# Optimization experiments

Measured on AMD Instinct MI355X. Metric: run time of the kernel, lower is better.

## Reference

```python
import jax, jax.numpy as jnp
import numpy as np

MARGIN = 0.2


def setup_inputs() -> dict:
    key = jax.random.key(0)
    ks = jax.random.split(key, 6)
    B, E = 8192, 1024
    return {
        "A_is_t": jax.random.normal(ks[0], (B, E), dtype=jnp.float32),
        "A_em_t": jax.random.normal(ks[1], (B, E), dtype=jnp.float32),
        "m": jax.random.normal(ks[2], (B, E), dtype=jnp.float32),
        "tr_m": jax.random.normal(ks[3], (B, E), dtype=jnp.float32),
        "W": jax.random.normal(ks[4], (E, E), dtype=jnp.float32) * (1.0 / np.sqrt(E)),
        "b": jax.random.normal(ks[5], (E,), dtype=jnp.float32) * 0.01,
    }


def reference(A_is_t, A_em_t, m, tr_m, W, b):
    # Linear layer: w(A) = A @ W.T + b  (torch nn.Linear convention)
    wA_is = A_is_t @ W.T + b  # [B, E]
    wA_em = A_em_t @ W.T + b  # [B, E]
    # Original builds full [B,B] score matrices but only uses the diagonal;
    # diagonal entries are exactly rowwise dots, computed directly here.
    d_is = jnp.einsum("be,be->b", m, wA_is)
    d_em = jnp.einsum("be,be->b", m, wA_em)
    d_is_trm = jnp.einsum("be,be->b", tr_m, wA_is)
    d_em_trm = jnp.einsum("be,be->b", tr_m, wA_em)
    diag_is_all = 0.4 * d_is + 0.6 * d_is_trm  # [B]
    diag_em_all = 0.6 * d_em_trm + 0.4 * d_em  # [B]
    cost_s = jnp.maximum(MARGIN + diag_is_all - diag_em_all, 0.0)  # hinge
    return cost_s.reshape(-1, 1).sum(axis=0)  # [1], matches cost_s.sum(0)
```

## Files before the change

kernel.cpp:

```cpp
#include <hip/hip_runtime.h>
#include <hip/hip_bf16.h>

#define B_ROWS 8192
#define E_DIM  1024
#define MARGIN 0.2f

#define BM 128
#define BN 128
#define BK 32
#define NSTEPS (E_DIM / BK)

typedef __bf16 bf16x8 __attribute__((ext_vector_type(8)));
typedef float  f32x4  __attribute__((ext_vector_type(4)));

__device__ __forceinline__ void gload_lds16(const void* g, void* l) {
    __builtin_amdgcn_global_load_lds(
        (__attribute__((address_space(1))) void*)(g),
        (__attribute__((address_space(3))) void*)(l),
        16, 0, 0);
}

#define GATE4() do { asm volatile("s_waitcnt vmcnt(4)" ::: "memory"); \
                     __builtin_amdgcn_sched_barrier(0); } while (0)
#define GATE0() do { asm volatile("s_waitcnt vmcnt(0)" ::: "memory"); \
                     __builtin_amdgcn_sched_barrier(0); } while (0)
#define RBAR()  do { __builtin_amdgcn_s_barrier(); \
                     __builtin_amdgcn_sched_barrier(0); } while (0)
#define LGKM0() do { asm volatile("s_waitcnt lgkmcnt(0)" ::: "memory"); \
                     __builtin_amdgcn_sched_barrier(0); } while (0)

__global__ __launch_bounds__(256)
void prep_combo(const float* __restrict__ m, const float* __restrict__ trm,
                __bf16* __restrict__ c,
                const float* __restrict__ W, __bf16* __restrict__ Wt) {
    __shared__ float tile[32][33];
    if (blockIdx.x < 4096) {
        size_t i = ((size_t)blockIdx.x * blockDim.x + threadIdx.x) * 8;
        float4 m0 = *(const float4*)(m + i);
        float4 m1 = *(const float4*)(m + i + 4);
        float4 t0 = *(const float4*)(trm + i);
        float4 t1 = *(const float4*)(trm + i + 4);
        bf16x8 v;
        v[0] = (__bf16)(0.4f*m0.x + 0.6f*t0.x);
        v[1] = (__bf16)(0.4f*m0.y + 0.6f*t0.y);
        v[2] = (__bf16)(0.4f*m0.z + 0.6f*t0.z);
        v[3] = (__bf16)(0.4f*m0.w + 0.6f*t0.w);
        v[4] = (__bf16)(0.4f*m1.x + 0.6f*t1.x);
        v[5] = (__bf16)(0.4f*m1.y + 0.6f*t1.y);
        v[6] = (__bf16)(0.4f*m1.z + 0.6f*t1.z);
        v[7] = (__bf16)(0.4f*m1.w + 0.6f*t1.w);
        *(bf16x8*)(c + i) = v;
    } else {
        const int tb = blockIdx.x - 4096;
        const int bx = (tb & 31) * 32;
        const int by = (tb >> 5) * 32;
        const int tx = threadIdx.x & 31;
        const int ty0 = threadIdx.x >> 5;
#pragma unroll
        for (int r = 0; r < 32; r += 8)
            tile[r + ty0][tx] = W[(size_t)(by + r + ty0) * E_DIM + bx + tx];
        __syncthreads();
#pragma unroll
        for (int r = 0; r < 32; r += 8)
            Wt[(size_t)(bx + r + ty0) * E_DIM + by + tx] = (__bf16)tile[tx][r + ty0];
    }
}

__global__ __launch_bounds__(256)
void gemm_dot(const __bf16* __restrict__ Cm, const __bf16* __restrict__ Wt,
              const float* __restrict__ Ais, const float* __restrict__ Aem,
              float* __restrict__ delta) {
    __shared__ __bf16 As[3][BM * BK];
    __shared__ __bf16 Bs[3][BN * BK];

    const int tid  = threadIdx.x;
    const int lane = tid & 63;
    const int wave = tid >> 6;
    const int lr   = lane & 15;
    const int hi   = lane >> 4;
    const int wr   = wave >> 1, wc = wave & 1;

    const int bid  = blockIdx.x;
    const int xcd  = bid & 7;
    const int q    = bid >> 3;
    const int rb   = (xcd * 8 + (q >> 3)) * BM;
    const int cb   = (q & 7) * BN;

    auto stage = [&](int slot, int k0) {
#pragma unroll
        for (int i = 0; i < 2; ++i) {
            int off = i * 4096 + tid * 16;
            int row = off >> 6;
            int kb  = off & 63;
            gload_lds16((const char*)Cm + ((size_t)(rb + row) * E_DIM + k0) * 2 + kb,
                        (char*)(&As[slot][0]) + off);
            gload_lds16((const char*)Wt + ((size_t)(cb + row) * E_DIM + k0) * 2 + kb,
                        (char*)(&Bs[slot][0]) + off);
        }
    };

    f32x4 acc[4][4] = {};

    stage(0, 0);
    stage(1, BK);

    int s0 = 0, s1 = 1, s2 = 2;
    for (int t = 0; t < NSTEPS; ++t) {
        if (t + 1 < NSTEPS) GATE4(); else GATE0();
        RBAR();

        bf16x8 a[4], b[4];
#pragma unroll
        for (int mi = 0; mi < 4; ++mi)
            a[mi] = *(const bf16x8*)(&As[s0][(wr * 64 + mi * 16 + lr) * BK + hi * 8]);
#pragma unroll
        for (int ni = 0; ni < 4; ++ni)
            b[ni] = *(const bf16x8*)(&Bs[s0][(wc * 64 + ni * 16 + lr) * BK + hi * 8]);
        LGKM0();

        if (t + 2 < NSTEPS) stage(s2, (t + 2) * BK);

        __builtin_amdgcn_s_setprio(1);
#pragma unroll
        for (int mi = 0; mi < 4; ++mi)
#pragma unroll
            for (int ni = 0; ni < 4; ++ni)
                acc[mi][ni] = __builtin_amdgcn_mfma_f32_16x16x32_bf16(
                    a[mi], b[ni], acc[mi][ni], 0, 0, 0);
        __builtin_amdgcn_s_setprio(0);

        int tmp = s0; s0 = s1; s1 = s2; s2 = tmp;
    }

    const int colbase = cb + wc * 64 + lr;
    const int rowbase = rb + wr * 64 + hi * 4;
#pragma unroll
    for (int mi = 0; mi < 4; ++mi) {
#pragma unroll
        for (int jj = 0; jj < 4; ++jj) {
            const int r = rowbase + mi * 16 + jj;
            float v = 0.f;
#pragma unroll
            for (int ni = 0; ni < 4; ++ni) {
                const size_t idx = (size_t)r * E_DIM + colbase + ni * 16;
                v += acc[mi][ni][jj] * (Ais[idx] - Aem[idx]);
            }
            v += __shfl_xor(v, 1);
            v += __shfl_xor(v, 2);
            v += __shfl_xor(v, 4);
            v += __shfl_xor(v, 8);
            if (lr == 0) atomicAdd(&delta[r], v);
        }
    }
}

__global__ void hinge_sum(const float* __restrict__ delta, float* __restrict__ out) {
    float s = 0.f;
    for (int i = threadIdx.x; i < B_ROWS; i += 256)
        s += fmaxf(MARGIN + delta[i], 0.f);
#pragma unroll
    for (int off = 32; off > 0; off >>= 1) s += __shfl_down(s, off);
    __shared__ float wsum[4];
    int lane = threadIdx.x & 63, w = threadIdx.x >> 6;
    if (lane == 0) wsum[w] = s;
    __syncthreads();
    if (threadIdx.x == 0) out[0] = wsum[0] + wsum[1] + wsum[2] + wsum[3];
}

extern "C" void kernel_launch(void* const* d_in, const int* in_sizes, int n_in,
                              void* d_out, int out_size, void* d_ws, size_t ws_size,
                              hipStream_t stream) {
    const float* A_is = (const float*)d_in[0];
    const float* A_em = (const float*)d_in[1];
    const float* m    = (const float*)d_in[2];
    const float* tr_m = (const float*)d_in[3];
    const float* W    = (const float*)d_in[4];
    float* out = (float*)d_out;

    char* ws = (char*)d_ws;
    __bf16* c     = (__bf16*)ws;
    __bf16* wt    = (__bf16*)(ws + (size_t)16 * 1024 * 1024);
    float*  delta = (float*) (ws + (size_t)18 * 1024 * 1024);

    hipMemsetAsync(delta, 0, B_ROWS * sizeof(float), stream);
    prep_combo<<<5120, 256, 0, stream>>>(m, tr_m, c, W, wt);
    gemm_dot<<<512, 256, 0, stream>>>(c, wt, A_is, A_em, delta);
    hinge_sum<<<1, 256, 0, stream>>>(delta, out);
}
```

Before: 61.23 us.

## Split K in two for gemm_dot and stage accumulators through LDS for coalesced epilogue

The GEMM reduction dimension is split into two halves, so the grid doubles to 1024 blocks, each covering half of K for a 128x128 tile. Partial dot contributions combine through the existing atomicAdd into delta. The epilogue now writes the accumulator tile to LDS as bf16, then reads A_is/A_em with row-contiguous float4 loads and reduces across 32 lanes. This aims at more occupancy and latency hiding, and at better-coalesced epilogue loads. The cost is that each A_is/A_em tile is read twice (once per K half), atomics double, and the intermediate product is rounded to bf16.

```diff
diff --git a/kernel.cpp b/kernel.cpp
--- a/kernel.cpp
+++ b/kernel.cpp
@@ -8,9 +8,12 @@
 #define BM 128
 #define BN 128
 #define BK 32
-#define NSTEPS (E_DIM / BK)
+#define KSPLIT 2
+#define KHALF (E_DIM / KSPLIT)
+#define NSTEPS (KHALF / BK)
 
 typedef __bf16 bf16x8 __attribute__((ext_vector_type(8)));
+typedef __bf16 bf16x4 __attribute__((ext_vector_type(4)));
 typedef float  f32x4  __attribute__((ext_vector_type(4)));
 
 __device__ __forceinline__ void gload_lds16(const void* g, void* l) {
@@ -70,8 +73,9 @@
 void gemm_dot(const __bf16* __restrict__ Cm, const __bf16* __restrict__ Wt,
               const float* __restrict__ Ais, const float* __restrict__ Aem,
               float* __restrict__ delta) {
-    __shared__ __bf16 As[3][BM * BK];
-    __shared__ __bf16 Bs[3][BN * BK];
+    __shared__ char smem[49152];
+    __bf16* Asb = (__bf16*)smem;
+    __bf16* Bsb = (__bf16*)(smem + 24576);
 
     const int tid  = threadIdx.x;
     const int lane = tid & 63;
@@ -80,11 +84,12 @@
     const int hi   = lane >> 4;
     const int wr   = wave >> 1, wc = wave & 1;
 
-    const int bid  = blockIdx.x;
-    const int xcd  = bid & 7;
-    const int q    = bid >> 3;
-    const int rb   = (xcd * 8 + (q >> 3)) * BM;
-    const int cb   = (q & 7) * BN;
+    const int bid = blockIdx.x;
+    const int xcd = bid & 7;
+    const int q   = bid >> 3;
+    const int rb    = (xcd * 8 + (q >> 4)) * BM;
+    const int cb    = (q & 7) * BN;
+    const int kbase = ((q >> 3) & 1) * KHALF;
 
     auto stage = [&](int slot, int k0) {
 #pragma unroll
@@ -93,16 +98,16 @@
             int row = off >> 6;
             int kb  = off & 63;
             gload_lds16((const char*)Cm + ((size_t)(rb + row) * E_DIM + k0) * 2 + kb,
-                        (char*)(&As[slot][0]) + off);
+                        smem + slot * 8192 + off);
             gload_lds16((const char*)Wt + ((size_t)(cb + row) * E_DIM + k0) * 2 + kb,
-                        (char*)(&Bs[slot][0]) + off);
+                        smem + 24576 + slot * 8192 + off);
         }
     };
 
     f32x4 acc[4][4] = {};
 
-    stage(0, 0);
-    stage(1, BK);
+    stage(0, kbase);
+    stage(1, kbase + BK);
 
     int s0 = 0, s1 = 1, s2 = 2;
     for (int t = 0; t < NSTEPS; ++t) {
@@ -112,13 +117,13 @@
         bf16x8 a[4], b[4];
 #pragma unroll
         for (int mi = 0; mi < 4; ++mi)
-            a[mi] = *(const bf16x8*)(&As[s0][(wr * 64 + mi * 16 + lr) * BK + hi * 8]);
+            a[mi] = *(const bf16x8*)(&Asb[s0 * 4096 + (wr * 64 + mi * 16 + lr) * BK + hi * 8]);
 #pragma unroll
         for (int ni = 0; ni < 4; ++ni)
-            b[ni] = *(const bf16x8*)(&Bs[s0][(wc * 64 + ni * 16 + lr) * BK + hi * 8]);
+            b[ni] = *(const bf16x8*)(&Bsb[s0 * 4096 + (wc * 64 + ni * 16 + lr) * BK + hi * 8]);
         LGKM0();
 
-        if (t + 2 < NSTEPS) stage(s2, (t + 2) * BK);
+        if (t + 2 < NSTEPS) stage(s2, kbase + (t + 2) * BK);
 
         __builtin_amdgcn_s_setprio(1);
 #pragma unroll
@@ -132,25 +137,41 @@
         int tmp = s0; s0 = s1; s1 = s2; s2 = tmp;
     }
 
-    const int colbase = cb + wc * 64 + lr;
-    const int rowbase = rb + wr * 64 + hi * 4;
-#pragma unroll
-    for (int mi = 0; mi < 4; ++mi) {
+    __syncthreads();
+    __bf16* u_lds = (__bf16*)smem;
+
+    const int rloc0 = wr * 64 + hi * 4;
+    const int cloc0 = wc * 64 + lr;
+#pragma unroll
+    for (int mi = 0; mi < 4; ++mi)
 #pragma unroll
         for (int jj = 0; jj < 4; ++jj) {
-            const int r = rowbase + mi * 16 + jj;
-            float v = 0.f;
-#pragma unroll
-            for (int ni = 0; ni < 4; ++ni) {
-                const size_t idx = (size_t)r * E_DIM + colbase + ni * 16;
-                v += acc[mi][ni][jj] * (Ais[idx] - Aem[idx]);
-            }
-            v += __shfl_xor(v, 1);
-            v += __shfl_xor(v, 2);
-            v += __shfl_xor(v, 4);
-            v += __shfl_xor(v, 8);
-            if (lr == 0) atomicAdd(&delta[r], v);
+            __bf16* row = u_lds + (rloc0 + mi * 16 + jj) * 128 + cloc0;
+#pragma unroll
+            for (int ni = 0; ni < 4; ++ni)
+                row[ni * 16] = (__bf16)acc[mi][ni][jj];
         }
+    __syncthreads();
+
+    const int half = lane >> 5;
+    const int cloc = (lane & 31) * 4;
+#pragma unroll 4
+    for (int it = 0; it < 16; ++it) {
+        const int rloc = wave * 32 + it * 2 + half;
+        const size_t gidx = (size_t)(rb + rloc) * E_DIM + cb + cloc;
+        const float4 ai = *(const float4*)(Ais + gidx);
+        const float4 ae = *(const float4*)(Aem + gidx);
+        const bf16x4 u4 = *(const bf16x4*)(u_lds + rloc * 128 + cloc);
+        float s = (float)u4[0] * (ai.x - ae.x)
+                + (float)u4[1] * (ai.y - ae.y)
+                + (float)u4[2] * (ai.z - ae.z)
+                + (float)u4[3] * (ai.w - ae.w);
+        s += __shfl_xor(s, 1);
+        s += __shfl_xor(s, 2);
+        s += __shfl_xor(s, 4);
+        s += __shfl_xor(s, 8);
+        s += __shfl_xor(s, 16);
+        if ((lane & 31) == 0) atomicAdd(&delta[rb + rloc], s);
     }
 }
 
@@ -184,6 +205,6 @@
 
     hipMemsetAsync(delta, 0, B_ROWS * sizeof(float), stream);
     prep_combo<<<5120, 256, 0, stream>>>(m, tr_m, c, W, wt);
-    gemm_dot<<<512, 256, 0, stream>>>(c, wt, A_is, A_em, delta);
+    gemm_dot<<<1024, 256, 0, stream>>>(c, wt, A_is, A_em, delta);
     hinge_sum<<<1, 256, 0, stream>>>(delta, out);
 }
```

New measurement: 70.19 us. 14.6% more time.

## Use 256x256 tiles with split-K, 8 waves, swizzled LDS and staged pipeline

Applied to the files above, without the earlier changes.

Restructures the GEMM into 256x256 output tiles computed by 8-wave blocks, with the K dimension split in two across blocks so the grid stays at 256 blocks. LDS tiles are XOR-swizzled to avoid bank conflicts, and global-to-LDS loads are issued in four interleaved sub-groups per K step, double buffered. The aim is more operand reuse per loaded byte and better overlap of loads with MFMA work. In exchange each thread holds twice as many accumulators, which raises register pressure, and split-K doubles the atomic traffic in the epilogue.

```diff
diff --git a/kernel.cpp b/kernel.cpp
--- a/kernel.cpp
+++ b/kernel.cpp
@@ -5,10 +5,12 @@
 #define E_DIM  1024
 #define MARGIN 0.2f
 
-#define BM 128
-#define BN 128
-#define BK 32
-#define NSTEPS (E_DIM / BK)
+#define BM 256
+#define BN 256
+#define BK 64
+#define KSPLIT 2
+#define KHALF (E_DIM / KSPLIT)
+#define NT (KHALF / BK)
 
 typedef __bf16 bf16x8 __attribute__((ext_vector_type(8)));
 typedef float  f32x4  __attribute__((ext_vector_type(4)));
@@ -20,7 +22,7 @@
         16, 0, 0);
 }
 
-#define GATE4() do { asm volatile("s_waitcnt vmcnt(4)" ::: "memory"); \
+#define GATE6() do { asm volatile("s_waitcnt vmcnt(6)" ::: "memory"); \
                      __builtin_amdgcn_sched_barrier(0); } while (0)
 #define GATE0() do { asm volatile("s_waitcnt vmcnt(0)" ::: "memory"); \
                      __builtin_amdgcn_sched_barrier(0); } while (0)
@@ -66,90 +68,157 @@
     }
 }
 
-__global__ __launch_bounds__(256)
+__global__ __launch_bounds__(512, 2)
 void gemm_dot(const __bf16* __restrict__ Cm, const __bf16* __restrict__ Wt,
               const float* __restrict__ Ais, const float* __restrict__ Aem,
               float* __restrict__ delta) {
-    __shared__ __bf16 As[3][BM * BK];
-    __shared__ __bf16 Bs[3][BN * BK];
+    __shared__ __bf16 AU[2][4][2][2048];
+    __shared__ __bf16 BU[2][4][2][2048];
 
     const int tid  = threadIdx.x;
     const int lane = tid & 63;
-    const int wave = tid >> 6;
     const int lr   = lane & 15;
     const int hi   = lane >> 4;
-    const int wr   = wave >> 1, wc = wave & 1;
-
-    const int bid  = blockIdx.x;
-    const int xcd  = bid & 7;
-    const int q    = bid >> 3;
-    const int rb   = (xcd * 8 + (q >> 3)) * BM;
-    const int cb   = (q & 7) * BN;
-
-    auto stage = [&](int slot, int k0) {
-#pragma unroll
-        for (int i = 0; i < 2; ++i) {
-            int off = i * 4096 + tid * 16;
-            int row = off >> 6;
-            int kb  = off & 63;
-            gload_lds16((const char*)Cm + ((size_t)(rb + row) * E_DIM + k0) * 2 + kb,
-                        (char*)(&As[slot][0]) + off);
-            gload_lds16((const char*)Wt + ((size_t)(cb + row) * E_DIM + k0) * 2 + kb,
-                        (char*)(&Bs[slot][0]) + off);
+    const int wave = tid >> 6;
+    const int wr   = wave >> 2;
+    const int wc   = wave & 3;
+
+    const int bid   = blockIdx.x;
+    const int xcd   = bid & 7;
+    const int loc   = bid >> 3;
+    const int panel = xcd * 4 + (loc >> 3);
+    const int sub   = loc & 7;
+    const int rb    = panel * BM;
+    const int cb    = (sub & 3) * BN;
+    const int kbase = (sub >> 2) * KHALF;
+
+    auto stageUnit = [&](int isA, int q, int kk, int T) {
+        const int d   = (tid & 255) * 16;
+        const int row = d >> 6;
+        const int x   = (d & 63) ^ (((row >> 1) & 3) << 4);
+        const char* g = (const char*)(isA ? Cm : Wt) +
+            ((size_t)((isA ? rb : cb) + q * 64 + row) * E_DIM +
+             kbase + T * BK + kk * 32) * 2 + x;
+        char* l = (char*)(isA ? &AU[T & 1][q][kk][0] : &BU[T & 1][q][kk][0]) + d;
+        gload_lds16(g, l);
+    };
+
+    auto stage_group = [&](int s, int T) {
+        switch (s) {
+        case 0: stageUnit(1, 2 * wr, 0, T);     stageUnit(1, 2 * wr, 1, T);     break;
+        case 1: stageUnit(0, wr, 0, T);         stageUnit(1, 2 * wr + 1, 0, T); break;
+        case 2: stageUnit(0, wr + 2, 0, T);     stageUnit(0, wr, 1, T);         break;
+        default: stageUnit(1, 2 * wr + 1, 1, T); stageUnit(0, wr + 2, 1, T);    break;
         }
     };
 
-    f32x4 acc[4][4] = {};
-
-    stage(0, 0);
-    stage(1, BK);
-
-    int s0 = 0, s1 = 1, s2 = 2;
-    for (int t = 0; t < NSTEPS; ++t) {
-        if (t + 1 < NSTEPS) GATE4(); else GATE0();
+    auto rdA = [&](int buf, int q, int kk, int ml) -> bf16x8 {
+        const int row  = ml * 16 + lr;
+        const int byte = row * 64 + ((hi * 16) ^ (((row >> 1) & 3) << 4));
+        return *(const bf16x8*)((const char*)&AU[buf][q][kk][0] + byte);
+    };
+    auto rdB = [&](int buf, int kk, int ni) -> bf16x8 {
+        const int row  = ni * 16 + lr;
+        const int byte = row * 64 + ((hi * 16) ^ (((row >> 1) & 3) << 4));
+        return *(const bf16x8*)((const char*)&BU[buf][wc][kk][0] + byte);
+    };
+
+    f32x4 acc[8][4] = {};
+    bf16x8 b0[4], b1[4];
+
+    stage_group(0, 0); stage_group(1, 0); stage_group(2, 0); stage_group(3, 0);
+
+    for (int p = 0; p <= 4 * NT + 1; ++p) {
+        if (p <= 4 * NT - 5) stage_group(p & 3, (p >> 2) + 1);
+
+        const int e = p - 2;
+        if (e >= 0 && e < 4 * NT) {
+            const int t = e >> 2, buf = t & 1, j = e & 3;
+            bf16x8 a[4];
+            switch (j) {
+            case 0:
+#pragma unroll
+                for (int ml = 0; ml < 4; ++ml) a[ml] = rdA(buf, 2 * wr, 0, ml);
+#pragma unroll
+                for (int ni = 0; ni < 4; ++ni) b0[ni] = rdB(buf, 0, ni);
+                LGKM0();
+                __builtin_amdgcn_s_setprio(1);
+#pragma unroll
+                for (int ml = 0; ml < 4; ++ml)
+#pragma unroll
+                    for (int ni = 0; ni < 4; ++ni)
+                        acc[ml][ni] = __builtin_amdgcn_mfma_f32_16x16x32_bf16(
+                            a[ml], b0[ni], acc[ml][ni], 0, 0, 0);
+                __builtin_amdgcn_s_setprio(0);
+                break;
+            case 1:
+#pragma unroll
+                for (int ml = 0; ml < 4; ++ml) a[ml] = rdA(buf, 2 * wr, 1, ml);
+#pragma unroll
+                for (int ni = 0; ni < 4; ++ni) b1[ni] = rdB(buf, 1, ni);
+                LGKM0();
+                __builtin_amdgcn_s_setprio(1);
+#pragma unroll
+                for (int ml = 0; ml < 4; ++ml)
+#pragma unroll
+                    for (int ni = 0; ni < 4; ++ni)
+                        acc[ml][ni] = __builtin_amdgcn_mfma_f32_16x16x32_bf16(
+                            a[ml], b1[ni], acc[ml][ni], 0, 0, 0);
+                __builtin_amdgcn_s_setprio(0);
+                break;
+            case 2:
+#pragma unroll
+                for (int ml = 0; ml < 4; ++ml) a[ml] = rdA(buf, 2 * wr + 1, 0, ml);
+                LGKM0();
+                __builtin_amdgcn_s_setprio(1);
+#pragma unroll
+                for (int ml = 0; ml < 4; ++ml)
+#pragma unroll
+                    for (int ni = 0; ni < 4; ++ni)
+                        acc[4 + ml][ni] = __builtin_amdgcn_mfma_f32_16x16x32_bf16(
+                            a[ml], b0[ni], acc[4 + ml][ni], 0, 0, 0);
+                __builtin_amdgcn_s_setprio(0);
+                break;
+            default:
+#pragma unroll
+                for (int ml = 0; ml < 4; ++ml) a[ml] = rdA(buf, 2 * wr + 1, 1, ml);
+                LGKM0();
+                __builtin_amdgcn_s_setprio(1);
+#pragma unroll
+                for (int ml = 0; ml < 4; ++ml)
+#pragma unroll
+                    for (int ni = 0; ni < 4; ++ni)
+                        acc[4 + ml][ni] = __builtin_amdgcn_mfma_f32_16x16x32_bf16(
+                            a[ml], b1[ni], acc[4 + ml][ni], 0, 0, 0);
+                __builtin_amdgcn_s_setprio(0);
+                break;
+            }
+        }
+
+        if (p <= 4 * NT - 5) { GATE6(); } else { GATE0(); }
         RBAR();
-
-        bf16x8 a[4], b[4];
-#pragma unroll
-        for (int mi = 0; mi < 4; ++mi)
-            a[mi] = *(const bf16x8*)(&As[s0][(wr * 64 + mi * 16 + lr) * BK + hi * 8]);
-#pragma unroll
-        for (int ni = 0; ni < 4; ++ni)
-            b[ni] = *(const bf16x8*)(&Bs[s0][(wc * 64 + ni * 16 + lr) * BK + hi * 8]);
-        LGKM0();
-
-        if (t + 2 < NSTEPS) stage(s2, (t + 2) * BK);
-
-        __builtin_amdgcn_s_setprio(1);
-#pragma unroll
-        for (int mi = 0; mi < 4; ++mi)
-#pragma unroll
-            for (int ni = 0; ni < 4; ++ni)
-                acc[mi][ni] = __builtin_amdgcn_mfma_f32_16x16x32_bf16(
-                    a[mi], b[ni], acc[mi][ni], 0, 0, 0);
-        __builtin_amdgcn_s_setprio(0);
-
-        int tmp = s0; s0 = s1; s1 = s2; s2 = tmp;
     }
 
     const int colbase = cb + wc * 64 + lr;
-    const int rowbase = rb + wr * 64 + hi * 4;
-#pragma unroll
-    for (int mi = 0; mi < 4; ++mi) {
-#pragma unroll
-        for (int jj = 0; jj < 4; ++jj) {
-            const int r = rowbase + mi * 16 + jj;
-            float v = 0.f;
-#pragma unroll
-            for (int ni = 0; ni < 4; ++ni) {
-                const size_t idx = (size_t)r * E_DIM + colbase + ni * 16;
-                v += acc[mi][ni][jj] * (Ais[idx] - Aem[idx]);
+#pragma unroll
+    for (int mh = 0; mh < 2; ++mh) {
+#pragma unroll
+        for (int ml = 0; ml < 4; ++ml) {
+#pragma unroll
+            for (int jj = 0; jj < 4; ++jj) {
+                const int r = rb + (2 * wr + mh) * 64 + ml * 16 + hi * 4 + jj;
+                float v = 0.f;
+#pragma unroll
+                for (int ni = 0; ni < 4; ++ni) {
+                    const size_t idx = (size_t)r * E_DIM + colbase + ni * 16;
+                    v += acc[mh * 4 + ml][ni][jj] * (Ais[idx] - Aem[idx]);
+                }
+                v += __shfl_xor(v, 1);
+                v += __shfl_xor(v, 2);
+                v += __shfl_xor(v, 4);
+                v += __shfl_xor(v, 8);
+                if (lr == 0) atomicAdd(&delta[r], v);
             }
-            v += __shfl_xor(v, 1);
-            v += __shfl_xor(v, 2);
-            v += __shfl_xor(v, 4);
-            v += __shfl_xor(v, 8);
-            if (lr == 0) atomicAdd(&delta[r], v);
         }
     }
 }
@@ -184,6 +253,6 @@
 
     hipMemsetAsync(delta, 0, B_ROWS * sizeof(float), stream);
     prep_combo<<<5120, 256, 0, stream>>>(m, tr_m, c, W, wt);
-    gemm_dot<<<512, 256, 0, stream>>>(c, wt, A_is, A_em, delta);
+    gemm_dot<<<256, 512, 0, stream>>>(c, wt, A_is, A_em, delta);
     hinge_sum<<<1, 256, 0, stream>>>(delta, out);
 }
```

Measured after the change: 78.57 us. +28.3%, slower.

## Fuse m/tr_m combination into GEMM A-tile load and drop prep pass

Applied to the files above, without the earlier changes.

The separate pass that blended m and tr_m into a bf16 buffer is removed. The GEMM now streams fp32 m and tr_m tiles straight into swizzled LDS, blends and converts them to bf16 while building the MFMA operands, and switches from a 3-stage to a 2-stage buffer with __syncthreads. The memset is folded into the W-transpose kernel, which saves one launch and the intermediate write and read of 16MB. The cost is more global and LDS traffic inside the GEMM (fp32 A read for each of the 8 column blocks) and a shallower pipeline with full barriers.

```diff
diff --git a/kernel.cpp b/kernel.cpp
--- a/kernel.cpp
+++ b/kernel.cpp
@@ -20,38 +20,12 @@
         16, 0, 0);
 }
 
-#define GATE4() do { asm volatile("s_waitcnt vmcnt(4)" ::: "memory"); \
-                     __builtin_amdgcn_sched_barrier(0); } while (0)
-#define GATE0() do { asm volatile("s_waitcnt vmcnt(0)" ::: "memory"); \
-                     __builtin_amdgcn_sched_barrier(0); } while (0)
-#define RBAR()  do { __builtin_amdgcn_s_barrier(); \
-                     __builtin_amdgcn_sched_barrier(0); } while (0)
-#define LGKM0() do { asm volatile("s_waitcnt lgkmcnt(0)" ::: "memory"); \
-                     __builtin_amdgcn_sched_barrier(0); } while (0)
-
 __global__ __launch_bounds__(256)
-void prep_combo(const float* __restrict__ m, const float* __restrict__ trm,
-                __bf16* __restrict__ c,
-                const float* __restrict__ W, __bf16* __restrict__ Wt) {
-    __shared__ float tile[32][33];
-    if (blockIdx.x < 4096) {
-        size_t i = ((size_t)blockIdx.x * blockDim.x + threadIdx.x) * 8;
-        float4 m0 = *(const float4*)(m + i);
-        float4 m1 = *(const float4*)(m + i + 4);
-        float4 t0 = *(const float4*)(trm + i);
-        float4 t1 = *(const float4*)(trm + i + 4);
-        bf16x8 v;
-        v[0] = (__bf16)(0.4f*m0.x + 0.6f*t0.x);
-        v[1] = (__bf16)(0.4f*m0.y + 0.6f*t0.y);
-        v[2] = (__bf16)(0.4f*m0.z + 0.6f*t0.z);
-        v[3] = (__bf16)(0.4f*m0.w + 0.6f*t0.w);
-        v[4] = (__bf16)(0.4f*m1.x + 0.6f*t1.x);
-        v[5] = (__bf16)(0.4f*m1.y + 0.6f*t1.y);
-        v[6] = (__bf16)(0.4f*m1.z + 0.6f*t1.z);
-        v[7] = (__bf16)(0.4f*m1.w + 0.6f*t1.w);
-        *(bf16x8*)(c + i) = v;
-    } else {
-        const int tb = blockIdx.x - 4096;
+void trans_zero(const float* __restrict__ W, __bf16* __restrict__ Wt,
+                float* __restrict__ delta) {
+    if (blockIdx.x < 1024) {
+        __shared__ float tile[32][33];
+        const int tb = blockIdx.x;
         const int bx = (tb & 31) * 32;
         const int by = (tb >> 5) * 32;
         const int tx = threadIdx.x & 31;
@@ -63,15 +37,19 @@
 #pragma unroll
         for (int r = 0; r < 32; r += 8)
             Wt[(size_t)(bx + r + ty0) * E_DIM + by + tx] = (__bf16)tile[tx][r + ty0];
+    } else {
+        delta[(blockIdx.x - 1024) * 256 + threadIdx.x] = 0.f;
     }
 }
 
 __global__ __launch_bounds__(256)
-void gemm_dot(const __bf16* __restrict__ Cm, const __bf16* __restrict__ Wt,
-              const float* __restrict__ Ais, const float* __restrict__ Aem,
-              float* __restrict__ delta) {
-    __shared__ __bf16 As[3][BM * BK];
-    __shared__ __bf16 Bs[3][BN * BK];
+void gemm_fused(const float* __restrict__ mIn, const float* __restrict__ trmIn,
+                const __bf16* __restrict__ Wt,
+                const float* __restrict__ Ais, const float* __restrict__ Aem,
+                float* __restrict__ delta) {
+    __shared__ float  Ms[2][BM * BK];
+    __shared__ float  Ts[2][BM * BK];
+    __shared__ __bf16 Bs[2][BN * BK];
 
     const int tid  = threadIdx.x;
     const int lane = tid & 63;
@@ -80,56 +58,73 @@
     const int hi   = lane >> 4;
     const int wr   = wave >> 1, wc = wave & 1;
 
-    const int bid  = blockIdx.x;
-    const int xcd  = bid & 7;
-    const int q    = bid >> 3;
-    const int rb   = (xcd * 8 + (q >> 3)) * BM;
-    const int cb   = (q & 7) * BN;
+    const int bid = blockIdx.x;
+    const int xcd = bid & 7;
+    const int q   = bid >> 3;
+    const int rb  = (xcd * 8 + (q >> 3)) * BM;
+    const int cb  = (q & 7) * BN;
 
-    auto stage = [&](int slot, int k0) {
+    auto stage = [&](int buf, int k0) {
+#pragma unroll
+        for (int i = 0; i < 4; ++i) {
+            const int d   = i * 4096 + tid * 16;
+            const int row = d >> 7;
+            const int cbi = (d & 127) ^ ((row & 7) << 4);
+            const size_t g = ((size_t)(rb + row) * E_DIM + k0) * 4 + cbi;
+            gload_lds16((const char*)mIn + g,   (char*)(&Ms[buf][0]) + d);
+            gload_lds16((const char*)trmIn + g, (char*)(&Ts[buf][0]) + d);
+        }
 #pragma unroll
         for (int i = 0; i < 2; ++i) {
-            int off = i * 4096 + tid * 16;
-            int row = off >> 6;
-            int kb  = off & 63;
-            gload_lds16((const char*)Cm + ((size_t)(rb + row) * E_DIM + k0) * 2 + kb,
-                        (char*)(&As[slot][0]) + off);
+            const int d   = i * 4096 + tid * 16;
+            const int row = d >> 6;
+            const int kb  = d & 63;
             gload_lds16((const char*)Wt + ((size_t)(cb + row) * E_DIM + k0) * 2 + kb,
-                        (char*)(&Bs[slot][0]) + off);
+                        (char*)(&Bs[buf][0]) + d);
         }
     };
 
     f32x4 acc[4][4] = {};
 
     stage(0, 0);
-    stage(1, BK);
+    __syncthreads();
 
-    int s0 = 0, s1 = 1, s2 = 2;
+    int cur = 0;
     for (int t = 0; t < NSTEPS; ++t) {
-        if (t + 1 < NSTEPS) GATE4(); else GATE0();
-        RBAR();
+        if (t + 1 < NSTEPS) stage(cur ^ 1, (t + 1) * BK);
 
+        const char* mb = (const char*)&Ms[cur][0];
+        const char* tb = (const char*)&Ts[cur][0];
         bf16x8 a[4], b[4];
 #pragma unroll
-        for (int mi = 0; mi < 4; ++mi)
-            a[mi] = *(const bf16x8*)(&As[s0][(wr * 64 + mi * 16 + lr) * BK + hi * 8]);
+        for (int mi = 0; mi < 4; ++mi) {
+            const int row = wr * 64 + mi * 16 + lr;
+            const int s   = (row & 7) << 4;
+            const int o0  = row * 128 + ((hi * 32) ^ s);
+            const int o1  = row * 128 + ((hi * 32 + 16) ^ s);
+            const f32x4 m0 = *(const f32x4*)(mb + o0);
+            const f32x4 m1 = *(const f32x4*)(mb + o1);
+            const f32x4 t0 = *(const f32x4*)(tb + o0);
+            const f32x4 t1 = *(const f32x4*)(tb + o1);
+#pragma unroll
+            for (int j = 0; j < 4; ++j) {
+                a[mi][j]     = (__bf16)(0.4f * m0[j] + 0.6f * t0[j]);
+                a[mi][4 + j] = (__bf16)(0.4f * m1[j] + 0.6f * t1[j]);
+            }
+        }
 #pragma unroll
         for (int ni = 0; ni < 4; ++ni)
-            b[ni] = *(const bf16x8*)(&Bs[s0][(wc * 64 + ni * 16 + lr) * BK + hi * 8]);
-        LGKM0();
+            b[ni] = *(const bf16x8*)(&Bs[cur][(wc * 64 + ni * 16 + lr) * BK + hi * 8]);
 
-        if (t + 2 < NSTEPS) stage(s2, (t + 2) * BK);
-
-        __builtin_amdgcn_s_setprio(1);
 #pragma unroll
         for (int mi = 0; mi < 4; ++mi)
 #pragma unroll
             for (int ni = 0; ni < 4; ++ni)
                 acc[mi][ni] = __builtin_amdgcn_mfma_f32_16x16x32_bf16(
                     a[mi], b[ni], acc[mi][ni], 0, 0, 0);
-        __builtin_amdgcn_s_setprio(0);
 
-        int tmp = s0; s0 = s1; s1 = s2; s2 = tmp;
+        __syncthreads();
+        cur ^= 1;
     }
 
     const int colbase = cb + wc * 64 + lr;
@@ -178,12 +173,10 @@
     float* out = (float*)d_out;
 
     char* ws = (char*)d_ws;
-    __bf16* c     = (__bf16*)ws;
-    __bf16* wt    = (__bf16*)(ws + (size_t)16 * 1024 * 1024);
-    float*  delta = (float*) (ws + (size_t)18 * 1024 * 1024);
+    __bf16* wt    = (__bf16*)ws;
+    float*  delta = (float*)(ws + (size_t)2 * 1024 * 1024);
 
-    hipMemsetAsync(delta, 0, B_ROWS * sizeof(float), stream);
-    prep_combo<<<5120, 256, 0, stream>>>(m, tr_m, c, W, wt);
-    gemm_dot<<<512, 256, 0, stream>>>(c, wt, A_is, A_em, delta);
+    trans_zero<<<1056, 256, 0, stream>>>(W, wt, delta);
+    gemm_fused<<<512, 256, 0, stream>>>(m, tr_m, wt, A_is, A_em, delta);
     hinge_sum<<<1, 256, 0, stream>>>(delta, out);
 }
```

Measured after the change: 78.32 us. 1.28x slower.
